# Kernel optimization log

Hardware: AMD Instinct MI355X
Metric: run time of the kernel (lower is better)

## Reference

```python
import jax, jax.numpy as jnp
import numpy as np

N, E, D, R = 50000, 600000, 128, 8


def rgcn_conv(x, src, dst, etype, W, root, bias):
    """PyG-style RGCNConv with mean aggregation per relation.
    x: [N, Din]; W: [R, Din, Dout]; root: [Din, Dout]; bias: [Dout]."""
    n = x.shape[0]
    r = W.shape[0]
    # Transform once per relation at node level (cheaper than per-edge matmul).
    xw = jnp.einsum('nd,rdo->rno', x, W)  # [R, N, Dout]
    # Per-(relation, target) edge counts for mean normalization.
    seg = etype * n + dst                  # combined segment id in [0, R*N)
    counts = jax.ops.segment_sum(jnp.ones(src.shape, dtype=x.dtype), seg,
                                 num_segments=r * n)
    norm = 1.0 / jnp.maximum(counts[seg], 1.0)   # [E]
    msg = xw[etype, src] * norm[:, None]          # gather per edge, [E, Dout]
    agg = jax.ops.segment_sum(msg, dst, num_segments=n)  # scatter-add, [N, Dout]
    return agg + x @ root + bias


def setup_inputs() -> dict:
    key = jax.random.key(0)
    ks = jax.random.split(key, 16)
    s = 1.0 / np.sqrt(D)
    inp = {
        'x': jax.random.normal(ks[0], (N, D), dtype=jnp.float32),
        'edge_index': jax.random.randint(ks[1], (2, E), 0, N, dtype=jnp.int32),
        'edge_type': jax.random.randint(ks[2], (E,), 0, R, dtype=jnp.int32),
        'W1': jax.random.normal(ks[3], (R, D, D), dtype=jnp.float32) * s,
        'root1': jax.random.normal(ks[4], (D, D), dtype=jnp.float32) * s,
        'b1': jnp.zeros((D,), dtype=jnp.float32),
        'W2': jax.random.normal(ks[5], (R, D, D), dtype=jnp.float32) * s,
        'root2': jax.random.normal(ks[6], (D, D), dtype=jnp.float32) * s,
        'b2': jnp.zeros((D,), dtype=jnp.float32),
        'W3': jax.random.normal(ks[7], (R, D, D), dtype=jnp.float32) * s,
        'root3': jax.random.normal(ks[8], (D, D), dtype=jnp.float32) * s,
        'b3': jnp.zeros((D,), dtype=jnp.float32),
        'res_w': jax.random.normal(ks[9], (D, D), dtype=jnp.float32) * s,
        'res_b': jnp.zeros((D,), dtype=jnp.float32),
    }
    return inp


def reference(x, edge_index, edge_type, W1, root1, b1, W2, root2, b2,
              W3, root3, b3, res_w, res_b):
    src, dst = edge_index[0], edge_index[1]
    res = x @ res_w + res_b
    h = jax.nn.relu(rgcn_conv(x, src, dst, edge_type, W1, root1, b1))
    h = res + jax.nn.relu(h)
    h = jax.nn.relu(rgcn_conv(h, src, dst, edge_type, W2, root2, b2))
    h = res + jax.nn.relu(h)
    h = jax.nn.relu(rgcn_conv(h, src, dst, edge_type, W3, root3, b3))
    h = res + jax.nn.relu(h)
    # Dropout(0.05) is identity in eval mode.
    return h
```

## Files before the change

### kernel.cpp

```cpp
#include <hip/hip_runtime.h>
#include <hip/hip_bf16.h>

#define NN 50000
#define EE 600000
#define RR 8
#define NSEG (NN*RR)
#define NB_SCAN ((NSEG + 1023)/1024)

typedef unsigned int u32;
typedef __attribute__((ext_vector_type(8))) short bf16x8;
typedef __attribute__((ext_vector_type(4))) float f32x4;
typedef __attribute__((ext_vector_type(4))) u32 u32x4;

__device__ inline unsigned short f2bf(float f){
  u32 u = __float_as_uint(f);
  u32 r = (u + 0x7fffu + ((u >> 16) & 1u)) >> 16;
  return (unsigned short)r;
}
__device__ inline float bf2f(unsigned short b){ return __uint_as_float((u32)b << 16); }

#define GLD16(g, l)  __builtin_amdgcn_global_load_lds( \
    (const __attribute__((address_space(1))) void*)(g), \
    (__attribute__((address_space(3))) void*)(l), 16, 0, 0)

__global__ void cvt_k(const float* __restrict__ in, unsigned short* __restrict__ out, int n4){
  int i = blockIdx.x * 256 + threadIdx.x;
  if (i >= n4) return;
  float4 v = ((const float4*)in)[i];
  ushort4 o;
  o.x = f2bf(v.x); o.y = f2bf(v.y); o.z = f2bf(v.z); o.w = f2bf(v.w);
  ((ushort4*)out)[i] = o;
}

__global__ void pack_k(const float* __restrict__ Wrel, const float* __restrict__ root,
                       short* __restrict__ Bp, int nk32, int krel){
  int tid = blockIdx.x * 256 + threadIdx.x;
  if (tid >= nk32 * 512) return;
  int lane = tid & 63;
  int nf   = (tid >> 6) & 7;
  int k32  = tid >> 9;
  int col  = nf * 16 + (lane & 15);
  short vals[8];
#pragma unroll
  for (int i = 0; i < 8; ++i){
    int kk = k32 * 32 + ((lane >> 4) << 3) + i;
    float f = (kk < krel) ? Wrel[(size_t)kk * 128 + col]
                          : root[(size_t)(kk - krel) * 128 + col];
    vals[i] = (short)f2bf(f);
  }
  *(bf16x8*)(Bp + (size_t)tid * 8) = *(const bf16x8*)vals;
}

__global__ void count_k(const int* __restrict__ dst, const int* __restrict__ et,
                        u32* __restrict__ cnt){
  int e = blockIdx.x * 256 + threadIdx.x;
  if (e >= EE) return;
  atomicAdd(&cnt[(size_t)et[e] * NN + dst[e]], 1u);
}

__global__ void scan1_k(const u32* __restrict__ cnt, u32* __restrict__ offs, u32* __restrict__ bsum){
  __shared__ u32 s[512];
  int t = threadIdx.x;
  int base = blockIdx.x * 1024 + t * 4;
  u32 loc[4]; u32 sum = 0;
#pragma unroll
  for (int i = 0; i < 4; ++i){ loc[i] = (base + i < NSEG) ? cnt[base + i] : 0u; sum += loc[i]; }
  int pb = 0;
  s[t] = sum; __syncthreads();
  for (int off = 1; off < 256; off <<= 1){
    u32 v = s[pb * 256 + t];
    if (t >= off) v += s[pb * 256 + t - off];
    s[(pb ^ 1) * 256 + t] = v; pb ^= 1; __syncthreads();
  }
  u32 incl = s[pb * 256 + t];
  u32 excl = incl - sum;
  if (t == 255) bsum[blockIdx.x] = incl;
  u32 run = excl;
#pragma unroll
  for (int i = 0; i < 4; ++i){ if (base + i < NSEG) offs[base + i] = run; run += loc[i]; }
}

__global__ void scan2_k(u32* __restrict__ bsum){
  __shared__ u32 s[1024];
  int t = threadIdx.x;
  u32 v = (t < NB_SCAN) ? bsum[t] : 0u;
  int pb = 0;
  s[t] = v; __syncthreads();
  for (int off = 1; off < 512; off <<= 1){
    u32 x = s[pb * 512 + t];
    if (t >= off) x += s[pb * 512 + t - off];
    s[(pb ^ 1) * 512 + t] = x; pb ^= 1; __syncthreads();
  }
  u32 incl = s[pb * 512 + t];
  if (t < NB_SCAN) bsum[t] = incl - v;
}

__global__ void scan3_k(u32* __restrict__ offs, const u32* __restrict__ bsum){
  int t = threadIdx.x;
  int base = blockIdx.x * 1024 + t * 4;
  u32 add = bsum[blockIdx.x];
#pragma unroll
  for (int i = 0; i < 4; ++i){ if (base + i < NSEG) offs[base + i] += add; }
  if (blockIdx.x == 0 && t == 0) offs[NSEG] = EE;
}

__global__ void fill_k(const int* __restrict__ src, const int* __restrict__ dst,
                       const int* __restrict__ et, const u32* __restrict__ offs,
                       u32* __restrict__ cnt, int* __restrict__ elist){
  int e = blockIdx.x * 256 + threadIdx.x;
  if (e >= EE) return;
  int s = et[e] * NN + dst[e];
  u32 p = atomicSub(&cnt[s], 1u);
  elist[offs[s] + p - 1] = src[e];
}

#define ACC1(P0, P1) do{ \
  _Pragma("unroll") \
  for (int i_ = 0; i_ < 4; ++i_){ \
    s[2*i_]     += __uint_as_float((P0)[i_] << 16); \
    s[2*i_+1]   += __uint_as_float((P0)[i_] & 0xffff0000u); \
    s[8+2*i_]   += __uint_as_float((P1)[i_] << 16); \
    s[8+2*i_+1] += __uint_as_float((P1)[i_] & 0xffff0000u); \
  } }while(0)

__launch_bounds__(256, 6)
__global__ void agg_k(const u32* __restrict__ offs, const int* __restrict__ elist,
                      const unsigned short* __restrict__ h, unsigned short* __restrict__ a){
  int t = threadIdx.x;
  int g = t >> 3, ll8 = t & 7;
  int seg = blockIdx.x * 32 + g;
  u32 beg = offs[seg], end = offs[seg + 1];
  float s[16];
#pragma unroll
  for (int i = 0; i < 16; ++i) s[i] = 0.f;
  const unsigned short* hb = h + (size_t)ll8 * 16;
  u32 e = beg;
  for (; e + 4 <= end; e += 4){
    int s0 = elist[e], s1 = elist[e+1], s2 = elist[e+2], s3 = elist[e+3];
    const unsigned short* r0 = hb + (size_t)s0 * 128;
    const unsigned short* r1 = hb + (size_t)s1 * 128;
    const unsigned short* r2 = hb + (size_t)s2 * 128;
    const unsigned short* r3 = hb + (size_t)s3 * 128;
    u32x4 p00 = *(const u32x4*)r0, p01 = *(const u32x4*)(r0 + 8);
    u32x4 p10 = *(const u32x4*)r1, p11 = *(const u32x4*)(r1 + 8);
    u32x4 p20 = *(const u32x4*)r2, p21 = *(const u32x4*)(r2 + 8);
    u32x4 p30 = *(const u32x4*)r3, p31 = *(const u32x4*)(r3 + 8);
    ACC1(p00, p01); ACC1(p10, p11); ACC1(p20, p21); ACC1(p30, p31);
  }
  if (e + 2 <= end){
    int s0 = elist[e], s1 = elist[e+1];
    const unsigned short* r0 = hb + (size_t)s0 * 128;
    const unsigned short* r1 = hb + (size_t)s1 * 128;
    u32x4 p00 = *(const u32x4*)r0, p01 = *(const u32x4*)(r0 + 8);
    u32x4 p10 = *(const u32x4*)r1, p11 = *(const u32x4*)(r1 + 8);
    ACC1(p00, p01); ACC1(p10, p11);
    e += 2;
  }
  if (e < end){
    int s0 = elist[e];
    const unsigned short* r0 = hb + (size_t)s0 * 128;
    u32x4 p00 = *(const u32x4*)r0, p01 = *(const u32x4*)(r0 + 8);
    ACC1(p00, p01);
  }
  u32 deg = end - beg;
  if (deg){
    float inv = 1.f / (float)deg;
#pragma unroll
    for (int i = 0; i < 16; ++i) s[i] *= inv;
  }
  u32x4 o0, o1;
#pragma unroll
  for (int i = 0; i < 4; ++i){
    o0[i] = (u32)f2bf(s[2*i])   | ((u32)f2bf(s[2*i+1])   << 16);
    o1[i] = (u32)f2bf(s[8+2*i]) | ((u32)f2bf(s[8+2*i+1]) << 16);
  }
  unsigned short* ap = a + (size_t)seg * 128 + ll8 * 16;
  *(u32x4*)ap = o0;
  *(u32x4*)(ap + 8) = o1;
}

__launch_bounds__(256, 4)
__global__ void resg_k(const unsigned short* __restrict__ xb, const short* __restrict__ Bp,
                       const float* __restrict__ rb, unsigned short* __restrict__ resb){
  const int tid = threadIdx.x;
  const int w = tid >> 6, l = tid & 63;
  const int sub = l >> 4, llr = l & 15;
  const int rowbase = blockIdx.x * 64 + w * 16;
  int vr = rowbase + llr; if (vr > NN - 1) vr = NN - 1;
  f32x4 acc[8] = {};
#pragma unroll
  for (int t = 0; t < 4; ++t){
    bf16x8 af = *(const bf16x8*)(xb + (size_t)vr * 128 + (t * 4 + sub) * 8);
    const short* bb = Bp + (size_t)(t * 8) * 512 + l * 8;
#pragma unroll
    for (int nf = 0; nf < 8; ++nf){
      bf16x8 bq = *(const bf16x8*)(bb + nf * 512);
      acc[nf] = __builtin_amdgcn_mfma_f32_16x16x32_bf16(af, bq, acc[nf], 0, 0, 0);
    }
  }
  const int lr = l >> 4, lc = l & 15;
#pragma unroll
  for (int nf = 0; nf < 8; ++nf){
    int col = nf * 16 + lc;
    float bv = rb[col];
#pragma unroll
    for (int r = 0; r < 4; ++r){
      int row = rowbase + lr * 4 + r;
      if (row < NN) resb[(size_t)row * 128 + col] = f2bf(acc[nf][r] + bv);
    }
  }
}

template<int OUTMODE>
__launch_bounds__(256, 6)
__global__ void gemm_k(const unsigned short* __restrict__ Aa,
                       const unsigned short* __restrict__ Ah,
                       const short* __restrict__ Bp,
                       const float* __restrict__ bias,
                       const unsigned short* __restrict__ resb,
                       float* __restrict__ outf, unsigned short* __restrict__ outb){
  __shared__ short lds[10240];
  const int tid = threadIdx.x;
  const int w = tid >> 6, l = tid & 63;
  const int wm = w >> 1, wn = w & 1;
  const int sub = l >> 4, llr = l & 15;
  const int mbase = blockIdx.x * 32;
  const size_t plane = (size_t)NN * 128;
  f32x4 acc[4] = {};

  int arow = mbase + (l & 31); if (arow > NN - 1) arow = NN - 1;
  const int aq = w * 2 + (l >> 5);

#pragma unroll 1
  for (int kt = 0; kt < 18; ++kt){
    const unsigned short* abase = (kt < 16)
        ? Aa + (size_t)(kt >> 1) * plane + (size_t)(kt & 1) * 64
        : Ah + (size_t)(kt - 16) * 64;
    GLD16(abase + (size_t)arow * 128 + aq * 8, lds + (size_t)(w * 64) * 8);
    const short* bsrc = Bp + (size_t)kt * 8192;
#pragma unroll
    for (int i = 0; i < 4; ++i)
      GLD16(bsrc + (size_t)(i * 256 + tid) * 8, lds + (size_t)(2048 + (i * 256 + w * 64) * 8));
    __syncthreads();
#pragma unroll
    for (int t = 0; t < 2; ++t){
      bf16x8 af = *(const bf16x8*)(lds + (size_t)((t * 4 + sub) * 32 + wm * 16 + llr) * 8);
#pragma unroll
      for (int nf = 0; nf < 4; ++nf){
        bf16x8 bq = *(const bf16x8*)(lds + (size_t)(2048 + (t * 8 + wn * 4 + nf) * 512 + l * 8));
        acc[nf] = __builtin_amdgcn_mfma_f32_16x16x32_bf16(af, bq, acc[nf], 0, 0, 0);
      }
    }
    __syncthreads();
  }

  const int lr = l >> 4, lc = l & 15;
#pragma unroll
  for (int nf = 0; nf < 4; ++nf){
    int col = wn * 64 + nf * 16 + lc;
    float bv = bias[col];
#pragma unroll
    for (int r = 0; r < 4; ++r){
      int row = mbase + wm * 16 + lr * 4 + r;
      if (row < NN){
        float v = acc[nf][r] + bv;
        v = bf2f(resb[(size_t)row * 128 + col]) + fmaxf(v, 0.f);
        if (OUTMODE == 1) outb[(size_t)row * 128 + col] = f2bf(v);
        else              outf[(size_t)row * 128 + col] = v;
      }
    }
  }
}

extern "C" void kernel_launch(void* const* d_in, const int* in_sizes, int n_in,
                              void* d_out, int out_size, void* d_ws, size_t ws_size,
                              hipStream_t stream){
  const float* x  = (const float*)d_in[0];
  const int*   ei = (const int*)d_in[1];
  const int*   et = (const int*)d_in[2];
  const float* W1 = (const float*)d_in[3];
  const float* r1 = (const float*)d_in[4];
  const float* b1 = (const float*)d_in[5];
  const float* W2 = (const float*)d_in[6];
  const float* r2 = (const float*)d_in[7];
  const float* b2 = (const float*)d_in[8];
  const float* W3 = (const float*)d_in[9];
  const float* r3 = (const float*)d_in[10];
  const float* b3 = (const float*)d_in[11];
  const float* rw = (const float*)d_in[12];
  const float* rb = (const float*)d_in[13];
  const int* srcv = ei;
  const int* dstv = ei + EE;

  char* p = (char*)d_ws;
  auto take = [&](size_t b)->char*{ char* q = p; p += (b + 255) & ~(size_t)255; return q; };
  unsigned short* a    = (unsigned short*)take((size_t)NN * 1024 * 2);
  unsigned short* xb   = (unsigned short*)take((size_t)NN * 128 * 2);
  unsigned short* h1   = (unsigned short*)take((size_t)NN * 128 * 2);
  unsigned short* h2   = (unsigned short*)take((size_t)NN * 128 * 2);
  unsigned short* resb = (unsigned short*)take((size_t)NN * 128 * 2);
  short* Bp1 = (short*)take(36 * 4096 * 2);
  short* Bp2 = (short*)take(36 * 4096 * 2);
  short* Bp3 = (short*)take(36 * 4096 * 2);
  short* BpR = (short*)take(4 * 4096 * 2);
  u32* cnt   = (u32*)take((size_t)NSEG * 4);
  u32* offs  = (u32*)take((size_t)(NSEG + 1) * 4);
  int* elist = (int*)take((size_t)EE * 4);
  u32* bsum  = (u32*)take((size_t)NB_SCAN * 4);

  hipMemsetAsync(cnt, 0, (size_t)NSEG * 4, stream);

  cvt_k<<<(NN * 128 / 4 + 255) / 256, 256, 0, stream>>>(x, xb, NN * 128 / 4);
  pack_k<<<(36 * 512 + 255) / 256, 256, 0, stream>>>(W1, r1, Bp1, 36, 1024);
  pack_k<<<(36 * 512 + 255) / 256, 256, 0, stream>>>(W2, r2, Bp2, 36, 1024);
  pack_k<<<(36 * 512 + 255) / 256, 256, 0, stream>>>(W3, r3, Bp3, 36, 1024);
  pack_k<<<(4 * 512 + 255) / 256, 256, 0, stream>>>(nullptr, rw, BpR, 4, 0);

  count_k<<<(EE + 255) / 256, 256, 0, stream>>>(dstv, et, cnt);
  scan1_k<<<NB_SCAN, 256, 0, stream>>>(cnt, offs, bsum);
  scan2_k<<<1, 512, 0, stream>>>(bsum);
  scan3_k<<<NB_SCAN, 256, 0, stream>>>(offs, bsum);
  fill_k<<<(EE + 255) / 256, 256, 0, stream>>>(srcv, dstv, et, offs, cnt, elist);

  const int GB = (NN + 31) / 32;

  resg_k<<<(NN + 63) / 64, 256, 0, stream>>>(xb, BpR, rb, resb);

  agg_k<<<NSEG / 32, 256, 0, stream>>>(offs, elist, xb, a);
  gemm_k<1><<<GB, 256, 0, stream>>>(a, xb, Bp1, b1, resb, nullptr, h1);
  agg_k<<<NSEG / 32, 256, 0, stream>>>(offs, elist, h1, a);
  gemm_k<1><<<GB, 256, 0, stream>>>(a, h1, Bp2, b2, resb, nullptr, h2);
  agg_k<<<NSEG / 32, 256, 0, stream>>>(offs, elist, h2, a);
  gemm_k<2><<<GB, 256, 0, stream>>>(a, h2, Bp3, b3, resb, (float*)d_out, nullptr);
}
```

Measured before the change: 339.9 us.

## Double-buffer LDS in gemm_k to overlap next k-tile loads with MFMA

Splits the LDS tile in gemm_k into two buffers and issues the asynchronous global-to-LDS loads for tile k+1 before computing on tile k. Explicit vmcnt waits and raw barriers replace the plain __syncthreads. The goal is to hide global load latency behind the MFMA work. In exchange the kernel uses twice the LDS and the launch-bounds occupancy hint drops from 6 to 3 blocks, so fewer blocks can be resident per CU.

```diff
diff --git a/kernel.cpp b/kernel.cpp
--- a/kernel.cpp
+++ b/kernel.cpp
@@ -212,14 +212,14 @@
 }
 
 template<int OUTMODE>
-__launch_bounds__(256, 6)
+__launch_bounds__(256, 3)
 __global__ void gemm_k(const unsigned short* __restrict__ Aa,
                        const unsigned short* __restrict__ Ah,
                        const short* __restrict__ Bp,
                        const float* __restrict__ bias,
                        const unsigned short* __restrict__ resb,
                        float* __restrict__ outf, unsigned short* __restrict__ outb){
-  __shared__ short lds[10240];
+  __shared__ short lds[2][10240];
   const int tid = threadIdx.x;
   const int w = tid >> 6, l = tid & 63;
   const int wm = w >> 1, wn = w & 1;
@@ -231,28 +231,43 @@
   int arow = mbase + (l & 31); if (arow > NN - 1) arow = NN - 1;
   const int aq = w * 2 + (l >> 5);
 
-#pragma unroll 1
+#define STAGE(kt, b) do{ \
+    const unsigned short* abase_ = ((kt) < 16) \
+        ? Aa + (size_t)((kt) >> 1) * plane + (size_t)((kt) & 1) * 64 \
+        : Ah + (size_t)((kt) - 16) * 64; \
+    GLD16(abase_ + (size_t)arow * 128 + aq * 8, &lds[b][(size_t)(w * 64) * 8]); \
+    const short* bsrc_ = Bp + (size_t)(kt) * 8192; \
+    _Pragma("unroll") \
+    for (int i_ = 0; i_ < 4; ++i_) \
+      GLD16(bsrc_ + (size_t)(i_ * 256 + tid) * 8, \
+            &lds[b][(size_t)(2048 + (i_ * 256 + w * 64) * 8)]); \
+  }while(0)
+
+  STAGE(0, 0);
+
+#pragma unroll
   for (int kt = 0; kt < 18; ++kt){
-    const unsigned short* abase = (kt < 16)
-        ? Aa + (size_t)(kt >> 1) * plane + (size_t)(kt & 1) * 64
-        : Ah + (size_t)(kt - 16) * 64;
-    GLD16(abase + (size_t)arow * 128 + aq * 8, lds + (size_t)(w * 64) * 8);
-    const short* bsrc = Bp + (size_t)kt * 8192;
-#pragma unroll
-    for (int i = 0; i < 4; ++i)
-      GLD16(bsrc + (size_t)(i * 256 + tid) * 8, lds + (size_t)(2048 + (i * 256 + w * 64) * 8));
-    __syncthreads();
+    if (kt + 1 < 18) STAGE(kt + 1, (kt + 1) & 1);
+    __builtin_amdgcn_sched_barrier(0);
+    if (kt + 1 < 18) asm volatile("s_waitcnt vmcnt(5)" ::: "memory");
+    else             asm volatile("s_waitcnt vmcnt(0)" ::: "memory");
+    __builtin_amdgcn_sched_barrier(0);
+    __builtin_amdgcn_s_barrier();
+    const short* lb = lds[kt & 1];
 #pragma unroll
     for (int t = 0; t < 2; ++t){
-      bf16x8 af = *(const bf16x8*)(lds + (size_t)((t * 4 + sub) * 32 + wm * 16 + llr) * 8);
+      bf16x8 af = *(const bf16x8*)(lb + (size_t)((t * 4 + sub) * 32 + wm * 16 + llr) * 8);
 #pragma unroll
       for (int nf = 0; nf < 4; ++nf){
-        bf16x8 bq = *(const bf16x8*)(lds + (size_t)(2048 + (t * 8 + wn * 4 + nf) * 512 + l * 8));
+        bf16x8 bq = *(const bf16x8*)(lb + (size_t)(2048 + (t * 8 + wn * 4 + nf) * 512 + l * 8));
         acc[nf] = __builtin_amdgcn_mfma_f32_16x16x32_bf16(af, bq, acc[nf], 0, 0, 0);
       }
     }
-    __syncthreads();
-  }
+    asm volatile("s_waitcnt lgkmcnt(0)" ::: "memory");
+    __builtin_amdgcn_sched_barrier(0);
+    __builtin_amdgcn_s_barrier();
+  }
+#undef STAGE
 
   const int lr = l >> 4, lc = l & 15;
 #pragma unroll
```

After: 337.5 us. About the same (-0.7%).

## Fuse per-relation aggregation into GEMM via LDS-resident swizzled A tile

Applied to the files above, without the earlier changes.

Merges the aggregation kernel and the GEMM kernel into a single kernel per layer. Each 512-thread block gathers and averages neighbor features for its 32 nodes across all 8 relations plus the self row, then writes them into a 72 KB XOR-swizzled LDS tile. It then runs MFMA directly from that tile, loading B straight from global memory. This removes the round trip through the 100 MB intermediate `a` buffer and the per-k-step LDS staging and barriers. The cost is heavy LDS use per block, which limits occupancy, and uncached B loads from global memory.

```diff
diff --git a/kernel.cpp b/kernel.cpp
--- a/kernel.cpp
+++ b/kernel.cpp
@@ -114,71 +114,6 @@
   elist[offs[s] + p - 1] = src[e];
 }
 
-#define ACC1(P0, P1) do{ \
-  _Pragma("unroll") \
-  for (int i_ = 0; i_ < 4; ++i_){ \
-    s[2*i_]     += __uint_as_float((P0)[i_] << 16); \
-    s[2*i_+1]   += __uint_as_float((P0)[i_] & 0xffff0000u); \
-    s[8+2*i_]   += __uint_as_float((P1)[i_] << 16); \
-    s[8+2*i_+1] += __uint_as_float((P1)[i_] & 0xffff0000u); \
-  } }while(0)
-
-__launch_bounds__(256, 6)
-__global__ void agg_k(const u32* __restrict__ offs, const int* __restrict__ elist,
-                      const unsigned short* __restrict__ h, unsigned short* __restrict__ a){
-  int t = threadIdx.x;
-  int g = t >> 3, ll8 = t & 7;
-  int seg = blockIdx.x * 32 + g;
-  u32 beg = offs[seg], end = offs[seg + 1];
-  float s[16];
-#pragma unroll
-  for (int i = 0; i < 16; ++i) s[i] = 0.f;
-  const unsigned short* hb = h + (size_t)ll8 * 16;
-  u32 e = beg;
-  for (; e + 4 <= end; e += 4){
-    int s0 = elist[e], s1 = elist[e+1], s2 = elist[e+2], s3 = elist[e+3];
-    const unsigned short* r0 = hb + (size_t)s0 * 128;
-    const unsigned short* r1 = hb + (size_t)s1 * 128;
-    const unsigned short* r2 = hb + (size_t)s2 * 128;
-    const unsigned short* r3 = hb + (size_t)s3 * 128;
-    u32x4 p00 = *(const u32x4*)r0, p01 = *(const u32x4*)(r0 + 8);
-    u32x4 p10 = *(const u32x4*)r1, p11 = *(const u32x4*)(r1 + 8);
-    u32x4 p20 = *(const u32x4*)r2, p21 = *(const u32x4*)(r2 + 8);
-    u32x4 p30 = *(const u32x4*)r3, p31 = *(const u32x4*)(r3 + 8);
-    ACC1(p00, p01); ACC1(p10, p11); ACC1(p20, p21); ACC1(p30, p31);
-  }
-  if (e + 2 <= end){
-    int s0 = elist[e], s1 = elist[e+1];
-    const unsigned short* r0 = hb + (size_t)s0 * 128;
-    const unsigned short* r1 = hb + (size_t)s1 * 128;
-    u32x4 p00 = *(const u32x4*)r0, p01 = *(const u32x4*)(r0 + 8);
-    u32x4 p10 = *(const u32x4*)r1, p11 = *(const u32x4*)(r1 + 8);
-    ACC1(p00, p01); ACC1(p10, p11);
-    e += 2;
-  }
-  if (e < end){
-    int s0 = elist[e];
-    const unsigned short* r0 = hb + (size_t)s0 * 128;
-    u32x4 p00 = *(const u32x4*)r0, p01 = *(const u32x4*)(r0 + 8);
-    ACC1(p00, p01);
-  }
-  u32 deg = end - beg;
-  if (deg){
-    float inv = 1.f / (float)deg;
-#pragma unroll
-    for (int i = 0; i < 16; ++i) s[i] *= inv;
-  }
-  u32x4 o0, o1;
-#pragma unroll
-  for (int i = 0; i < 4; ++i){
-    o0[i] = (u32)f2bf(s[2*i])   | ((u32)f2bf(s[2*i+1])   << 16);
-    o1[i] = (u32)f2bf(s[8+2*i]) | ((u32)f2bf(s[8+2*i+1]) << 16);
-  }
-  unsigned short* ap = a + (size_t)seg * 128 + ll8 * 16;
-  *(u32x4*)ap = o0;
-  *(u32x4*)(ap + 8) = o1;
-}
-
 __launch_bounds__(256, 4)
 __global__ void resg_k(const unsigned short* __restrict__ xb, const short* __restrict__ Bp,
                        const float* __restrict__ rb, unsigned short* __restrict__ resb){
@@ -211,59 +146,127 @@
   }
 }
 
+#define ACC1(P0, P1) do{ \
+  _Pragma("unroll") \
+  for (int i_ = 0; i_ < 4; ++i_){ \
+    s[2*i_]     += __uint_as_float((P0)[i_] << 16); \
+    s[2*i_+1]   += __uint_as_float((P0)[i_] & 0xffff0000u); \
+    s[8+2*i_]   += __uint_as_float((P1)[i_] << 16); \
+    s[8+2*i_+1] += __uint_as_float((P1)[i_] & 0xffff0000u); \
+  } }while(0)
+
 template<int OUTMODE>
-__launch_bounds__(256, 6)
-__global__ void gemm_k(const unsigned short* __restrict__ Aa,
-                       const unsigned short* __restrict__ Ah,
-                       const short* __restrict__ Bp,
-                       const float* __restrict__ bias,
-                       const unsigned short* __restrict__ resb,
-                       float* __restrict__ outf, unsigned short* __restrict__ outb){
-  __shared__ short lds[10240];
+__launch_bounds__(512, 4)
+__global__ void fused_k(const u32* __restrict__ offs, const int* __restrict__ elist,
+                        const unsigned short* __restrict__ h,
+                        const short* __restrict__ Bp,
+                        const float* __restrict__ bias,
+                        const unsigned short* __restrict__ resb,
+                        float* __restrict__ outf, unsigned short* __restrict__ outb){
+  __shared__ short A[32 * 1152];
+  char* Ab = (char*)A;
   const int tid = threadIdx.x;
+  const int mbase = blockIdx.x * 32;
+
+  {
+    const int g = tid >> 3, ll8 = tid & 7;
+    const unsigned short* hb = h + (size_t)ll8 * 16;
+#pragma unroll 1
+    for (int j = 0; j < 5; ++j){
+      int task = j * 64 + g;
+      if (task < 256){
+        int r = task >> 5, row = task & 31;
+        int v = mbase + row; if (v > NN - 1) v = NN - 1;
+        size_t seg = (size_t)r * NN + v;
+        u32 beg = offs[seg], end = offs[seg + 1];
+        float s[16];
+#pragma unroll
+        for (int i = 0; i < 16; ++i) s[i] = 0.f;
+        u32 e = beg;
+        for (; e + 4 <= end; e += 4){
+          int s0 = elist[e], s1 = elist[e+1], s2 = elist[e+2], s3 = elist[e+3];
+          const unsigned short* r0 = hb + (size_t)s0 * 128;
+          const unsigned short* r1 = hb + (size_t)s1 * 128;
+          const unsigned short* r2 = hb + (size_t)s2 * 128;
+          const unsigned short* r3 = hb + (size_t)s3 * 128;
+          u32x4 p00 = *(const u32x4*)r0, p01 = *(const u32x4*)(r0 + 8);
+          u32x4 p10 = *(const u32x4*)r1, p11 = *(const u32x4*)(r1 + 8);
+          u32x4 p20 = *(const u32x4*)r2, p21 = *(const u32x4*)(r2 + 8);
+          u32x4 p30 = *(const u32x4*)r3, p31 = *(const u32x4*)(r3 + 8);
+          ACC1(p00, p01); ACC1(p10, p11); ACC1(p20, p21); ACC1(p30, p31);
+        }
+        if (e + 2 <= end){
+          int s0 = elist[e], s1 = elist[e+1];
+          const unsigned short* r0 = hb + (size_t)s0 * 128;
+          const unsigned short* r1 = hb + (size_t)s1 * 128;
+          u32x4 p00 = *(const u32x4*)r0, p01 = *(const u32x4*)(r0 + 8);
+          u32x4 p10 = *(const u32x4*)r1, p11 = *(const u32x4*)(r1 + 8);
+          ACC1(p00, p01); ACC1(p10, p11);
+          e += 2;
+        }
+        if (e < end){
+          int s0 = elist[e];
+          const unsigned short* r0 = hb + (size_t)s0 * 128;
+          u32x4 p00 = *(const u32x4*)r0, p01 = *(const u32x4*)(r0 + 8);
+          ACC1(p00, p01);
+        }
+        u32 deg = end - beg;
+        if (deg){
+          float inv = 1.f / (float)deg;
+#pragma unroll
+          for (int i = 0; i < 16; ++i) s[i] *= inv;
+        }
+        u32x4 o0, o1;
+#pragma unroll
+        for (int i = 0; i < 4; ++i){
+          o0[i] = (u32)f2bf(s[2*i])   | ((u32)f2bf(s[2*i+1])   << 16);
+          o1[i] = (u32)f2bf(s[8+2*i]) | ((u32)f2bf(s[8+2*i+1]) << 16);
+        }
+        int k = row & 7;
+        int sl = r * 16 + ll8 * 2;
+        *(u32x4*)(Ab + row * 2304 + ((sl    ) ^ k) * 16) = o0;
+        *(u32x4*)(Ab + row * 2304 + ((sl + 1) ^ k) * 16) = o1;
+      } else if (task < 288){
+        int row = task - 256;
+        int v = mbase + row; if (v > NN - 1) v = NN - 1;
+        const unsigned short* rp = h + (size_t)v * 128 + ll8 * 16;
+        u32x4 o0 = *(const u32x4*)rp, o1 = *(const u32x4*)(rp + 8);
+        int k = row & 7;
+        int sl = 128 + ll8 * 2;
+        *(u32x4*)(Ab + row * 2304 + ((sl    ) ^ k) * 16) = o0;
+        *(u32x4*)(Ab + row * 2304 + ((sl + 1) ^ k) * 16) = o1;
+      }
+    }
+  }
+  __syncthreads();
+
   const int w = tid >> 6, l = tid & 63;
-  const int wm = w >> 1, wn = w & 1;
   const int sub = l >> 4, llr = l & 15;
-  const int mbase = blockIdx.x * 32;
-  const size_t plane = (size_t)NN * 128;
-  f32x4 acc[4] = {};
-
-  int arow = mbase + (l & 31); if (arow > NN - 1) arow = NN - 1;
-  const int aq = w * 2 + (l >> 5);
-
-#pragma unroll 1
+  f32x4 acc[2] = {};
+  const int k0 = llr & 7, k1 = (16 + llr) & 7;
+#pragma unroll 6
   for (int kt = 0; kt < 18; ++kt){
-    const unsigned short* abase = (kt < 16)
-        ? Aa + (size_t)(kt >> 1) * plane + (size_t)(kt & 1) * 64
-        : Ah + (size_t)(kt - 16) * 64;
-    GLD16(abase + (size_t)arow * 128 + aq * 8, lds + (size_t)(w * 64) * 8);
-    const short* bsrc = Bp + (size_t)kt * 8192;
-#pragma unroll
-    for (int i = 0; i < 4; ++i)
-      GLD16(bsrc + (size_t)(i * 256 + tid) * 8, lds + (size_t)(2048 + (i * 256 + w * 64) * 8));
-    __syncthreads();
 #pragma unroll
     for (int t = 0; t < 2; ++t){
-      bf16x8 af = *(const bf16x8*)(lds + (size_t)((t * 4 + sub) * 32 + wm * 16 + llr) * 8);
-#pragma unroll
-      for (int nf = 0; nf < 4; ++nf){
-        bf16x8 bq = *(const bf16x8*)(lds + (size_t)(2048 + (t * 8 + wn * 4 + nf) * 512 + l * 8));
-        acc[nf] = __builtin_amdgcn_mfma_f32_16x16x32_bf16(af, bq, acc[nf], 0, 0, 0);
-      }
-    }
-    __syncthreads();
+      int ks = kt * 8 + t * 4 + sub;
+      bf16x8 af0 = *(const bf16x8*)(Ab + llr * 2304        + (ks ^ k0) * 16);
+      bf16x8 af1 = *(const bf16x8*)(Ab + (16 + llr) * 2304 + (ks ^ k1) * 16);
+      bf16x8 bq = *(const bf16x8*)(Bp + ((size_t)((kt * 2 + t) * 8 + w)) * 512 + l * 8);
+      acc[0] = __builtin_amdgcn_mfma_f32_16x16x32_bf16(af0, bq, acc[0], 0, 0, 0);
+      acc[1] = __builtin_amdgcn_mfma_f32_16x16x32_bf16(af1, bq, acc[1], 0, 0, 0);
+    }
   }
 
   const int lr = l >> 4, lc = l & 15;
-#pragma unroll
-  for (int nf = 0; nf < 4; ++nf){
-    int col = wn * 64 + nf * 16 + lc;
-    float bv = bias[col];
+  int col = w * 16 + lc;
+  float bv = bias[col];
+#pragma unroll
+  for (int mf = 0; mf < 2; ++mf){
 #pragma unroll
     for (int r = 0; r < 4; ++r){
-      int row = mbase + wm * 16 + lr * 4 + r;
+      int row = mbase + mf * 16 + lr * 4 + r;
       if (row < NN){
-        float v = acc[nf][r] + bv;
+        float v = acc[mf][r] + bv;
         v = bf2f(resb[(size_t)row * 128 + col]) + fmaxf(v, 0.f);
         if (OUTMODE == 1) outb[(size_t)row * 128 + col] = f2bf(v);
         else              outf[(size_t)row * 128 + col] = v;
@@ -294,7 +297,6 @@
 
   char* p = (char*)d_ws;
   auto take = [&](size_t b)->char*{ char* q = p; p += (b + 255) & ~(size_t)255; return q; };
-  unsigned short* a    = (unsigned short*)take((size_t)NN * 1024 * 2);
   unsigned short* xb   = (unsigned short*)take((size_t)NN * 128 * 2);
   unsigned short* h1   = (unsigned short*)take((size_t)NN * 128 * 2);
   unsigned short* h2   = (unsigned short*)take((size_t)NN * 128 * 2);
@@ -326,10 +328,7 @@
 
   resg_k<<<(NN + 63) / 64, 256, 0, stream>>>(xb, BpR, rb, resb);
 
-  agg_k<<<NSEG / 32, 256, 0, stream>>>(offs, elist, xb, a);
-  gemm_k<1><<<GB, 256, 0, stream>>>(a, xb, Bp1, b1, resb, nullptr, h1);
-  agg_k<<<NSEG / 32, 256, 0, stream>>>(offs, elist, h1, a);
-  gemm_k<1><<<GB, 256, 0, stream>>>(a, h1, Bp2, b2, resb, nullptr, h2);
-  agg_k<<<NSEG / 32, 256, 0, stream>>>(offs, elist, h2, a);
-  gemm_k<2><<<GB, 256, 0, stream>>>(a, h2, Bp3, b3, resb, (float*)d_out, nullptr);
-}
+  fused_k<1><<<GB, 512, 0, stream>>>(offs, elist, xb, Bp1, b1, resb, nullptr, h1);
+  fused_k<1><<<GB, 512, 0, stream>>>(offs, elist, h1, Bp2, b2, resb, nullptr, h2);
+  fused_k<2><<<GB, 512, 0, stream>>>(offs, elist, h2, Bp3, b3, resb, (float*)d_out, nullptr);
+}
```

Measured after the change: 316.6 us. -6.8%, faster.
